# Kernel tuning notes

Measured on AMD Instinct MI355X. Metric: run time of the kernel, lower is better.

Reference implementation:

```python
import jax, jax.numpy as jnp
import numpy as np
from jax import lax

B, MIN, DIN = 16, 8, 16
MOUT, DOUT = 8, 16
H, W = 32, 32
K, S, P, OP = 3, 2, 1, 1
NH, NW = 64, 64
ITERS = 2
EPS = 1e-7


def squash(s):
    # s: [..., D]; matches torch squash: factor * s / safe_norm
    sq = jnp.sum(s * s, axis=-1, keepdims=True)
    norm = jnp.sqrt(sq + EPS)
    return (sq / (1.0 + sq)) * s / norm


def setup_inputs() -> dict:
    key = jax.random.key(0)
    k1, k2, k3 = jax.random.split(key, 3)
    x = jax.random.normal(k1, (B, MIN, H, W, DIN), dtype=jnp.float32)
    # torch ConvTranspose2d weight layout: [in_ch, out_ch, kH, kW]
    w_deconv = jax.random.normal(k2, (MIN * DIN, MOUT * DOUT, K, K), dtype=jnp.float32) * 0.05
    b_deconv = jax.random.normal(k3, (MOUT * DOUT,), dtype=jnp.float32) * 0.05
    b_route = jnp.zeros((1, MOUT, NH, NW, MIN), dtype=jnp.float32)
    return {"x": x, "w_deconv": w_deconv, "b_deconv": b_deconv, "b_route": b_route}


def reference(x, w_deconv, b_deconv, b_route):
    Bb, Min, Hh, Ww, Din = x.shape
    # [B, Min, H, W, Din] -> [B, Min*Din, H, W]
    xc = jnp.transpose(x, (0, 1, 4, 2, 3)).reshape(Bb, Min * Din, Hh, Ww)
    # ConvTranspose2d == conv with lhs_dilation=stride and spatially-flipped, IO-swapped kernel
    wf = jnp.transpose(w_deconv, (1, 0, 2, 3))[:, :, ::-1, ::-1]  # [out, in, kH, kW]
    pad = (K - 1 - P, K - 1 - P + OP)
    y = lax.conv_general_dilated(
        xc, wf, window_strides=(1, 1), padding=[pad, pad],
        lhs_dilation=(S, S), dimension_numbers=("NCHW", "OIHW", "NCHW"))
    y = y + b_deconv[None, :, None, None]  # [B, Mout*Dout, NH, NW]
    nh, nw = y.shape[2], y.shape[3]
    # view([B, Mout, Dout, h, w, -1]).permute(0,1,3,4,5,2) -> [B, Mout, h, w, 1, Dout]
    pred = jnp.transpose(y.reshape(Bb, MOUT, DOUT, nh, nw, 1), (0, 1, 3, 4, 5, 2))
    # --- agreement routing ---
    c = jax.nn.softmax(b_route, axis=-1)                      # [1, Mout, h, w, Min]
    out = squash(jnp.sum(c[..., None] * pred, axis=-2))       # [B, Mout, h, w, Dout]
    b = b_route
    for _ in range(ITERS):
        b = b + jnp.sum(pred * out[..., None, :], axis=-1)    # [B, Mout, h, w, Min]
        c = jax.nn.softmax(b, axis=-1)
        out = squash(jnp.sum(pred * c[..., None], axis=-2))
    return out
```

## Files before the change

kernel.cpp:

```cpp
#include <hip/hip_runtime.h>
#include <hip/hip_bf16.h>
#include <math.h>


typedef __attribute__((ext_vector_type(8))) __bf16 bf16x8;
typedef __attribute__((ext_vector_type(4))) float f32x4;

#define XBF_ELEMS (16 * 8 * 32 * 32 * 16)

__global__ __launch_bounds__(256) void prep(const float* __restrict__ x,
                                            const float* __restrict__ w,
                                            __hip_bfloat16* __restrict__ xbf,
                                            __hip_bfloat16* __restrict__ wl) {
    const int bx = blockIdx.x;
    if (bx < 1024) {
        const int i = (bx * 256 + threadIdx.x) * 8;
        float4 a = *(const float4*)(x + i);
        float4 b = *(const float4*)(x + i + 4);
        union { bf16x8 v; __hip_bfloat162 h[4]; } u;
        u.h[0] = __float22bfloat162_rn(make_float2(a.x, a.y));
        u.h[1] = __float22bfloat162_rn(make_float2(a.z, a.w));
        u.h[2] = __float22bfloat162_rn(make_float2(b.x, b.y));
        u.h[3] = __float22bfloat162_rn(make_float2(b.z, b.w));
        *(bf16x8*)(xbf + i) = u.v;
    } else {
        const int idx = (bx - 1024) * 256 + threadIdx.x;
        const int ci  = idx / 1152;
        const int rem = idx - ci * 1152;
        const int co  = rem / 9;
        const int tap = rem - co * 9;
        const int s = ci >> 5, quad = (ci >> 3) & 3, j = ci & 7;
        const int t = co >> 4, n16 = co & 15;
        const int dst = ((((tap * 4 + s) * 8 + t) * 64) + quad * 16 + n16) * 8 + j;
        wl[dst] = __float2bfloat16(w[idx]);
    }
}

template <int PH, int PW>
__device__ __forceinline__ void caps_body(
    const __hip_bfloat16* __restrict__ xbf, const __hip_bfloat16* __restrict__ wl,
    const float* __restrict__ bias, float* __restrict__ out)
{
    const int tid = threadIdx.x, lane = tid & 63, wv = tid >> 6;
    const int q = blockIdx.y, b = blockIdx.z;
    const int rp = wv >> 1, ch = wv & 1;
    const int rw0 = q * 4 + rp * 2;
    const int n16  = lane & 15;
    const int quad = lane >> 4;
    const int c    = ch * 16 + n16;

    float bb[8];
    #pragma unroll
    for (int t = 0; t < 8; ++t) bb[t] = bias[t * 16 + n16];

    const __hip_bfloat16* xq = xbf + b * 131072 + (quad >> 1) * 16384 + (quad & 1) * 8;
    const __hip_bfloat16* wq = wl + lane * 8;

    f32x4 acc[2][8];
    #pragma unroll
    for (int r = 0; r < 2; ++r)
        #pragma unroll
        for (int t = 0; t < 8; ++t) acc[r][t] = (f32x4){0.f, 0.f, 0.f, 0.f};

    #pragma unroll
    for (int khi = 0; khi < (PH ? 2 : 1); ++khi) {
        const int kh = PH ? khi * 2 : 1;
        const int dh = PH ? (1 - khi) : 0;
        const int ih0 = rw0 + dh, ih1 = ih0 + 1;
        const bool v0 = (ih0 < 32), v1 = (ih1 < 32);
        const int ih0c = v0 ? ih0 : 31, ih1c = v1 ? ih1 : 31;
        #pragma unroll
        for (int kwi = 0; kwi < (PW ? 2 : 1); ++kwi) {
            const int kw = PW ? kwi * 2 : 1;
            const int dw = PW ? (1 - kwi) : 0;
            const int iw = c + dw;
            const bool vw = (iw < 32);
            const int iwc = vw ? iw : 31;
            const int tap = kh * 3 + kw;
            const __hip_bfloat16* a0p = xq + ih0c * 512 + iwc * 16;
            const __hip_bfloat16* a1p = xq + ih1c * 512 + iwc * 16;
            const __hip_bfloat16* wb  = wq + tap * 16384;
            #pragma unroll
            for (int s = 0; s < 4; ++s) {
                bf16x8 a0 = *(const bf16x8*)(a0p + s * 32768);
                bf16x8 a1 = *(const bf16x8*)(a1p + s * 32768);
                if (!(v0 && vw)) a0 = (bf16x8){};
                if (!(v1 && vw)) a1 = (bf16x8){};
                #pragma unroll
                for (int t = 0; t < 8; ++t) {
                    bf16x8 bf = *(const bf16x8*)(wb + (s * 8 + t) * 512);
                    acc[0][t] = __builtin_amdgcn_mfma_f32_16x16x32_bf16(a0, bf, acc[0][t], 0, 0, 0);
                    acc[1][t] = __builtin_amdgcn_mfma_f32_16x16x32_bf16(a1, bf, acc[1][t], 0, 0, 0);
                }
            }
        }
    }

    #pragma unroll
    for (int row = 0; row < 2; ++row) {
        const int oh = (rw0 + row) * 2 + PH;
        #pragma unroll
        for (int half = 0; half < 2; ++half) {
            float y[4][4], sq[4][4];
            #pragma unroll
            for (int tt = 0; tt < 4; ++tt)
                #pragma unroll
                for (int r = 0; r < 4; ++r) {
                    y[tt][r]  = acc[row][half * 4 + tt][r] + bb[half * 4 + tt];
                    sq[tt][r] = y[tt][r] * y[tt][r];
                }
            #pragma unroll
            for (int st = 1; st <= 8; st <<= 1)
                #pragma unroll
                for (int tt = 0; tt < 4; ++tt)
                    #pragma unroll
                    for (int r = 0; r < 4; ++r)
                        sq[tt][r] += __shfl_xor(sq[tt][r], st, 64);
            #pragma unroll
            for (int tt = 0; tt < 4; ++tt)
                #pragma unroll
                for (int r = 0; r < 4; ++r) {
                    const float s2 = sq[tt][r];
                    const float f  = s2 / ((1.f + s2) * sqrtf(s2 + 1e-7f));
                    const int ow = (ch * 16 + quad * 4 + r) * 2 + PW;
                    __builtin_nontemporal_store(
                        y[tt][r] * f,
                        out + (((b * 8 + half * 4 + tt) * 64 + oh) * 64 + ow) * 16 + n16);
                }
        }
    }
}

__global__ __launch_bounds__(256, 2) void caps_mfma(
    const __hip_bfloat16* __restrict__ xbf, const __hip_bfloat16* __restrict__ wl,
    const float* __restrict__ bias, float* __restrict__ out)
{
    switch (blockIdx.x) {
    case 0:  caps_body<0, 0>(xbf, wl, bias, out); break;
    case 1:  caps_body<0, 1>(xbf, wl, bias, out); break;
    case 2:  caps_body<1, 0>(xbf, wl, bias, out); break;
    default: caps_body<1, 1>(xbf, wl, bias, out); break;
    }
}

extern "C" void kernel_launch(void* const* d_in, const int* in_sizes, int n_in,
                              void* d_out, int out_size, void* d_ws, size_t ws_size,
                              hipStream_t stream) {
    const float* x    = (const float*)d_in[0];
    const float* wgt  = (const float*)d_in[1];
    const float* bias = (const float*)d_in[2];
    float* out = (float*)d_out;

    __hip_bfloat16* xbf = (__hip_bfloat16*)d_ws;
    __hip_bfloat16* wlb = xbf + XBF_ELEMS;

    prep<<<1024 + 576, 256, 0, stream>>>(x, wgt, xbf, wlb);
    caps_mfma<<<dim3(4, 8, 16), 256, 0, stream>>>(xbf, wlb, bias, out);
}
```

Before: 98.70 us.

## Split output capsules across two blocks to double grid and occupancy

Each block now computes only half of the output capsule types (4 of 8), selected by a new nh index taken from blockIdx.x, so the grid doubles from 512 to 1024 blocks. Accumulator registers are halved, which lets launch bounds move from 2 to 4 blocks per CU. The aim is more parallelism and better latency hiding on the MFMA loop. In exchange, each input tile is loaded twice, once by each block that shares it.

```diff
diff --git a/kernel.cpp b/kernel.cpp
--- a/kernel.cpp
+++ b/kernel.cpp
@@ -39,7 +39,7 @@
 template <int PH, int PW>
 __device__ __forceinline__ void caps_body(
     const __hip_bfloat16* __restrict__ xbf, const __hip_bfloat16* __restrict__ wl,
-    const float* __restrict__ bias, float* __restrict__ out)
+    const float* __restrict__ bias, float* __restrict__ out, int nh)
 {
     const int tid = threadIdx.x, lane = tid & 63, wv = tid >> 6;
     const int q = blockIdx.y, b = blockIdx.z;
@@ -49,18 +49,18 @@
     const int quad = lane >> 4;
     const int c    = ch * 16 + n16;
 
-    float bb[8];
+    float bb[4];
     #pragma unroll
-    for (int t = 0; t < 8; ++t) bb[t] = bias[t * 16 + n16];
+    for (int tt = 0; tt < 4; ++tt) bb[tt] = bias[(nh * 4 + tt) * 16 + n16];
 
     const __hip_bfloat16* xq = xbf + b * 131072 + (quad >> 1) * 16384 + (quad & 1) * 8;
-    const __hip_bfloat16* wq = wl + lane * 8;
+    const __hip_bfloat16* wq = wl + lane * 8 + (nh * 4) * 512;
 
-    f32x4 acc[2][8];
+    f32x4 acc[2][4];
     #pragma unroll
     for (int r = 0; r < 2; ++r)
         #pragma unroll
-        for (int t = 0; t < 8; ++t) acc[r][t] = (f32x4){0.f, 0.f, 0.f, 0.f};
+        for (int tt = 0; tt < 4; ++tt) acc[r][tt] = (f32x4){0.f, 0.f, 0.f, 0.f};
 
     #pragma unroll
     for (int khi = 0; khi < (PH ? 2 : 1); ++khi) {
@@ -87,10 +87,10 @@
                 if (!(v0 && vw)) a0 = (bf16x8){};
                 if (!(v1 && vw)) a1 = (bf16x8){};
                 #pragma unroll
-                for (int t = 0; t < 8; ++t) {
-                    bf16x8 bf = *(const bf16x8*)(wb + (s * 8 + t) * 512);
-                    acc[0][t] = __builtin_amdgcn_mfma_f32_16x16x32_bf16(a0, bf, acc[0][t], 0, 0, 0);
-                    acc[1][t] = __builtin_amdgcn_mfma_f32_16x16x32_bf16(a1, bf, acc[1][t], 0, 0, 0);
+                for (int tt = 0; tt < 4; ++tt) {
+                    bf16x8 bf = *(const bf16x8*)(wb + (s * 8 + tt) * 512);
+                    acc[0][tt] = __builtin_amdgcn_mfma_f32_16x16x32_bf16(a0, bf, acc[0][tt], 0, 0, 0);
+                    acc[1][tt] = __builtin_amdgcn_mfma_f32_16x16x32_bf16(a1, bf, acc[1][tt], 0, 0, 0);
                 }
             }
         }
@@ -99,47 +99,45 @@
     #pragma unroll
     for (int row = 0; row < 2; ++row) {
         const int oh = (rw0 + row) * 2 + PH;
+        float y[4][4], sq[4][4];
         #pragma unroll
-        for (int half = 0; half < 2; ++half) {
-            float y[4][4], sq[4][4];
+        for (int tt = 0; tt < 4; ++tt)
+            #pragma unroll
+            for (int r = 0; r < 4; ++r) {
+                y[tt][r]  = acc[row][tt][r] + bb[tt];
+                sq[tt][r] = y[tt][r] * y[tt][r];
+            }
+        #pragma unroll
+        for (int st = 1; st <= 8; st <<= 1)
             #pragma unroll
             for (int tt = 0; tt < 4; ++tt)
                 #pragma unroll
-                for (int r = 0; r < 4; ++r) {
-                    y[tt][r]  = acc[row][half * 4 + tt][r] + bb[half * 4 + tt];
-                    sq[tt][r] = y[tt][r] * y[tt][r];
-                }
+                for (int r = 0; r < 4; ++r)
+                    sq[tt][r] += __shfl_xor(sq[tt][r], st, 64);
+        #pragma unroll
+        for (int tt = 0; tt < 4; ++tt)
             #pragma unroll
-            for (int st = 1; st <= 8; st <<= 1)
-                #pragma unroll
-                for (int tt = 0; tt < 4; ++tt)
-                    #pragma unroll
-                    for (int r = 0; r < 4; ++r)
-                        sq[tt][r] += __shfl_xor(sq[tt][r], st, 64);
-            #pragma unroll
-            for (int tt = 0; tt < 4; ++tt)
-                #pragma unroll
-                for (int r = 0; r < 4; ++r) {
-                    const float s2 = sq[tt][r];
-                    const float f  = s2 / ((1.f + s2) * sqrtf(s2 + 1e-7f));
-                    const int ow = (ch * 16 + quad * 4 + r) * 2 + PW;
-                    __builtin_nontemporal_store(
-                        y[tt][r] * f,
-                        out + (((b * 8 + half * 4 + tt) * 64 + oh) * 64 + ow) * 16 + n16);
-                }
-        }
+            for (int r = 0; r < 4; ++r) {
+                const float s2 = sq[tt][r];
+                const float f  = s2 / ((1.f + s2) * sqrtf(s2 + 1e-7f));
+                const int ow = (ch * 16 + quad * 4 + r) * 2 + PW;
+                __builtin_nontemporal_store(
+                    y[tt][r] * f,
+                    out + (((b * 8 + nh * 4 + tt) * 64 + oh) * 64 + ow) * 16 + n16);
+            }
     }
 }
 
-__global__ __launch_bounds__(256, 2) void caps_mfma(
+__global__ __launch_bounds__(256, 4) void caps_mfma(
     const __hip_bfloat16* __restrict__ xbf, const __hip_bfloat16* __restrict__ wl,
     const float* __restrict__ bias, float* __restrict__ out)
 {
-    switch (blockIdx.x) {
-    case 0:  caps_body<0, 0>(xbf, wl, bias, out); break;
-    case 1:  caps_body<0, 1>(xbf, wl, bias, out); break;
-    case 2:  caps_body<1, 0>(xbf, wl, bias, out); break;
-    default: caps_body<1, 1>(xbf, wl, bias, out); break;
+    const int nh = blockIdx.x >> 2;
+    switch (blockIdx.x & 3) {
+    case 0:  caps_body<0, 0>(xbf, wl, bias, out, nh); break;
+    case 1:  caps_body<0, 1>(xbf, wl, bias, out, nh); break;
+    case 2:  caps_body<1, 0>(xbf, wl, bias, out, nh); break;
+    default: caps_body<1, 1>(xbf, wl, bias, out, nh); break;
     }
 }
 
@@ -155,5 +153,5 @@
     __hip_bfloat16* wlb = xbf + XBF_ELEMS;
 
     prep<<<1024 + 576, 256, 0, stream>>>(x, wgt, xbf, wlb);
-    caps_mfma<<<dim3(4, 8, 16), 256, 0, stream>>>(xbf, wlb, bias, out);
+    caps_mfma<<<dim3(8, 8, 16), 256, 0, stream>>>(xbf, wlb, bias, out);
 }
```

Result: faster. 94.66 us (-4.1%).
